# Optimization experiments

Measured on AMD Instinct MI355X. Metric: run time of the kernel, lower is better.

Reference implementation:

```python
import jax, jax.numpy as jnp
import numpy as np

K = 64          # number of instance ids (0 = background, skipped)
MARGIN = 1.0    # TripletMarginLoss margin
EPS = 1e-6      # torch pairwise_distance eps (added to the difference)
NCAND = 16      # random negative candidates per instance


def setup_inputs() -> dict:
    key = jax.random.key(0)
    k1, k2 = jax.random.split(key)
    sem_logits = jax.random.normal(k1, (4, 19, 1024, 1024), dtype=jnp.float32)
    instance_mask = jax.random.randint(k2, (1024, 1024), 0, K, dtype=jnp.int32)
    return {"sem_logits": sem_logits, "instance_mask": instance_mask}


def reference(sem_logits, instance_mask):
    B, C, H, W = sem_logits.shape
    HW = H * W
    sem_flat = sem_logits.reshape(B * C, HW)           # [BC, HW]
    mask_flat = instance_mask.reshape(HW)
    ar = jnp.arange(HW, dtype=jnp.int32)

    # first and second pixel (row-major order) of each instance id, vectorized
    first = jax.ops.segment_min(ar, mask_flat, num_segments=K)   # int32 max if empty
    ar2 = jnp.where(ar == first[mask_flat], jnp.int32(HW), ar)
    second = jax.ops.segment_min(ar2, mask_flat, num_segments=K)
    counts = jax.ops.segment_sum(jnp.ones_like(ar), mask_flat, num_segments=K)

    ids = jnp.arange(K, dtype=jnp.int32)
    valid = (counts >= 2) & (ids != 0)

    # random negative: first candidate pixel whose instance id differs
    cand = jax.random.randint(jax.random.key(1), (K, NCAND), 0, HW, dtype=jnp.int32)
    cand_ok = mask_flat[cand] != ids[:, None]
    pick = jnp.argmax(cand_ok, axis=1)
    neg = cand[jnp.arange(K), pick]

    f = jnp.clip(first, 0, HW - 1)
    s = jnp.clip(second, 0, HW - 1)

    a = sem_flat[:, f].T    # [K, B*C] anchor vectors (flattened per-pixel logits)
    p = sem_flat[:, s].T    # positive
    n = sem_flat[:, neg].T  # negative

    d_ap = jnp.linalg.norm(a - p + EPS, axis=1)
    d_an = jnp.linalg.norm(a - n + EPS, axis=1)
    per_inst = jnp.maximum(d_ap - d_an + MARGIN, 0.0)

    cnt = jnp.sum(valid)
    total = jnp.sum(jnp.where(valid, per_inst, 0.0))
    return jnp.where(cnt > 0, total / cnt, jnp.float32(0.0))
```

## Files before the change

### kernel.cpp

```cpp
#include <hip/hip_runtime.h>
#include <stdint.h>

#define HW        (1024 * 1024)
#define KIDS      64
#define NCANDS    16
#define BCC       76
#define EPSF      1e-6f
#define MARGINF   1.0f
#define SENTINEL  0x7FFFFFFF

#define JAX_PARTITIONABLE 1

__device__ __forceinline__ uint32_t rotl32(uint32_t v, int r) {
    return (v << r) | (v >> (32 - r));
}

__device__ void threefry2x32(uint32_t k0, uint32_t k1, uint32_t x0, uint32_t x1,
                             uint32_t* o0, uint32_t* o1) {
    const uint32_t ks2 = k0 ^ k1 ^ 0x1BD11BDAu;
    const int R0[4] = {13, 15, 26, 6};
    const int R1[4] = {17, 29, 16, 24};
    x0 += k0; x1 += k1;
#pragma unroll
    for (int i = 0; i < 4; i++) { x0 += x1; x1 = rotl32(x1, R0[i]); x1 ^= x0; }
    x0 += k1; x1 += ks2 + 1u;
#pragma unroll
    for (int i = 0; i < 4; i++) { x0 += x1; x1 = rotl32(x1, R1[i]); x1 ^= x0; }
    x0 += ks2; x1 += k0 + 2u;
#pragma unroll
    for (int i = 0; i < 4; i++) { x0 += x1; x1 = rotl32(x1, R0[i]); x1 ^= x0; }
    x0 += k0; x1 += k1 + 3u;
#pragma unroll
    for (int i = 0; i < 4; i++) { x0 += x1; x1 = rotl32(x1, R1[i]); x1 ^= x0; }
    x0 += k1; x1 += ks2 + 4u;
#pragma unroll
    for (int i = 0; i < 4; i++) { x0 += x1; x1 = rotl32(x1, R0[i]); x1 ^= x0; }
    x0 += ks2; x1 += k0 + 5u;
    *o0 = x0; *o1 = x1;
}

__device__ uint32_t jax_cand_bits(uint32_t j) {
#if JAX_PARTITIONABLE
    uint32_t k2a, k2b;
    threefry2x32(0u, 1u, 0u, 1u, &k2a, &k2b);
    uint32_t b1, b2;
    threefry2x32(k2a, k2b, 0u, j, &b1, &b2);
    return b1 ^ b2;
#else
    uint32_t a0, a1, b0, b1;
    threefry2x32(0u, 1u, 0u, 2u, &a0, &a1);
    threefry2x32(0u, 1u, 1u, 3u, &b0, &b1);
    uint32_t k2a = a1, k2b = b1;
    uint32_t r0, r1;
    if (j < 512u) { threefry2x32(k2a, k2b, j, j + 512u, &r0, &r1); return r0; }
    else          { threefry2x32(k2a, k2b, j - 512u, j, &r0, &r1); return r1; }
#endif
}

__global__ void k_init(int* g_first, int* g_second, int* g_count,
                       float* g_total, int* g_cnt) {
    int t = threadIdx.x;
    if (t < KIDS) { g_first[t] = SENTINEL; g_second[t] = SENTINEL; g_count[t] = 0; }
    if (t == 0)   { *g_total = 0.0f; *g_cnt = 0; }
}

__global__ void k_seg(const int* __restrict__ mask,
                      int* g_first, int* g_second, int* g_count) {
    __shared__ int m1[KIDS], m2[KIDS], cnt[KIDS];
    const int t = threadIdx.x;
    if (t < KIDS) { m1[t] = SENTINEL; m2[t] = SENTINEL; cnt[t] = 0; }
    __syncthreads();

    const int4* m4 = (const int4*)mask;
    const int base4 = blockIdx.x * 1024;
    int4 v[4];
#pragma unroll
    for (int c = 0; c < 4; c++) v[c] = m4[base4 + c * 256 + t];

#pragma unroll
    for (int c = 0; c < 4; c++) {
        const int pix0 = (base4 + c * 256 + t) * 4;
        const int ids[4] = {v[c].x, v[c].y, v[c].z, v[c].w};
#pragma unroll
        for (int j = 0; j < 4; j++) {
            atomicAdd(&cnt[ids[j]], 1);
            atomicMin(&m1[ids[j]], pix0 + j);
        }
    }
    __syncthreads();
#pragma unroll
    for (int c = 0; c < 4; c++) {
        const int pix0 = (base4 + c * 256 + t) * 4;
        const int ids[4] = {v[c].x, v[c].y, v[c].z, v[c].w};
#pragma unroll
        for (int j = 0; j < 4; j++) {
            if (pix0 + j != m1[ids[j]]) atomicMin(&m2[ids[j]], pix0 + j);
        }
    }
    __syncthreads();

    if (t < KIDS && cnt[t] > 0) {
        const int lm1 = m1[t];
        const int old = atomicMin(&g_first[t], lm1);
        const int disp = old > lm1 ? old : lm1;
        if (disp != SENTINEL)  atomicMin(&g_second[t], disp);
        if (m2[t] != SENTINEL) atomicMin(&g_second[t], m2[t]);
        atomicAdd(&g_count[t], cnt[t]);
    }
}

__global__ void k_triplet(const float* __restrict__ sem,
                          const int* __restrict__ mask,
                          const int* __restrict__ g_first,
                          const int* __restrict__ g_second,
                          const int* __restrict__ g_count,
                          float* g_total, int* g_cnt) {
    const int k = blockIdx.x;
    if (k == 0 || g_count[k] < 2) return;

    __shared__ int s_neg;
    __shared__ float red_ap[128], red_an[128];
    const int t = threadIdx.x;

    if (t == 0) {
        int neg = -1, first_cand = -1;
        for (int c = 0; c < NCANDS; c++) {
            const uint32_t bits = jax_cand_bits((uint32_t)(k * NCANDS + c));
            const int cand = (int)(bits & (uint32_t)(HW - 1));
            if (c == 0) first_cand = cand;
            if (neg < 0 && mask[cand] != k) neg = cand;
        }
        s_neg = (neg < 0) ? first_cand : neg;
    }
    __syncthreads();

    const int f = g_first[k], s = g_second[k], n = s_neg;
    float ap = 0.0f, an = 0.0f;
    if (t < BCC) {
        const size_t row = (size_t)t * (size_t)HW;
        const float a  = sem[row + f];
        const float p  = sem[row + s];
        const float nn = sem[row + n];
        const float d1 = a - p + EPSF;
        const float d2 = a - nn + EPSF;
        ap = d1 * d1;
        an = d2 * d2;
    }
    red_ap[t] = ap; red_an[t] = an;
    __syncthreads();
    for (int off = 64; off > 0; off >>= 1) {
        if (t < off) { red_ap[t] += red_ap[t + off]; red_an[t] += red_an[t + off]; }
        __syncthreads();
    }
    if (t == 0) {
        float per = sqrtf(red_ap[0]) - sqrtf(red_an[0]) + MARGINF;
        per = per > 0.0f ? per : 0.0f;
        atomicAdd(g_total, per);
        atomicAdd(g_cnt, 1);
    }
}

__global__ void k_final(const float* __restrict__ g_total,
                        const int* __restrict__ g_cnt, float* out) {
    const int c = *g_cnt;
    out[0] = (c > 0) ? (*g_total / (float)c) : 0.0f;
}

extern "C" void kernel_launch(void* const* d_in, const int* in_sizes, int n_in,
                              void* d_out, int out_size, void* d_ws, size_t ws_size,
                              hipStream_t stream) {
    const float* sem  = (const float*)d_in[0];
    const int*   mask = (const int*)d_in[1];
    float* out = (float*)d_out;

    int* ws = (int*)d_ws;
    int* g_first  = ws;
    int* g_second = ws + 64;
    int* g_count  = ws + 128;
    float* g_total = (float*)(ws + 192);
    int*   g_cnt   = ws + 193;

    k_init<<<1, 64, 0, stream>>>(g_first, g_second, g_count, g_total, g_cnt);
    k_seg<<<HW / 4096, 256, 0, stream>>>(mask, g_first, g_second, g_count);
    k_triplet<<<KIDS, 128, 0, stream>>>(sem, mask, g_first, g_second, g_count,
                                        g_total, g_cnt);
    k_final<<<1, 1, 0, stream>>>(g_total, g_cnt, out);
}
```

Measured before the change: 361.2 us.

## Replace global atomics with per-block partials and deterministic reductions, drop init kernel

The segment kernel now writes per-block (first, second) partial minima to workspace instead of doing global atomics and counts, so the separate init kernel can be removed. The triplet kernel merges the 256 partials per id with a two-smallest reduction, derives validity from the second index, and computes the 16 negative candidates in parallel with a wavefront ballot. The final kernel reduces per-id results with shuffles. This saves one launch and the global atomic contention, at the cost of a small extra reduction over the partials.

Measured after the change: 348.8 us. 3.4% less time.

```diff
diff --git a/kernel.cpp b/kernel.cpp
--- a/kernel.cpp
+++ b/kernel.cpp
@@ -8,6 +8,7 @@
 #define EPSF      1e-6f
 #define MARGINF   1.0f
 #define SENTINEL  0x7FFFFFFF
+#define SEGB      256
 
 #define JAX_PARTITIONABLE 1
 
@@ -57,18 +58,10 @@
 #endif
 }
 
-__global__ void k_init(int* g_first, int* g_second, int* g_count,
-                       float* g_total, int* g_cnt) {
-    int t = threadIdx.x;
-    if (t < KIDS) { g_first[t] = SENTINEL; g_second[t] = SENTINEL; g_count[t] = 0; }
-    if (t == 0)   { *g_total = 0.0f; *g_cnt = 0; }
-}
-
-__global__ void k_seg(const int* __restrict__ mask,
-                      int* g_first, int* g_second, int* g_count) {
-    __shared__ int m1[KIDS], m2[KIDS], cnt[KIDS];
+__global__ void k_seg(const int* __restrict__ mask, int2* __restrict__ part) {
+    __shared__ int m1[KIDS], m2[KIDS];
     const int t = threadIdx.x;
-    if (t < KIDS) { m1[t] = SENTINEL; m2[t] = SENTINEL; cnt[t] = 0; }
+    if (t < KIDS) { m1[t] = SENTINEL; m2[t] = SENTINEL; }
     __syncthreads();
 
     const int4* m4 = (const int4*)mask;
@@ -82,10 +75,7 @@
         const int pix0 = (base4 + c * 256 + t) * 4;
         const int ids[4] = {v[c].x, v[c].y, v[c].z, v[c].w};
 #pragma unroll
-        for (int j = 0; j < 4; j++) {
-            atomicAdd(&cnt[ids[j]], 1);
-            atomicMin(&m1[ids[j]], pix0 + j);
-        }
+        for (int j = 0; j < 4; j++) atomicMin(&m1[ids[j]], pix0 + j);
     }
     __syncthreads();
 #pragma unroll
@@ -99,42 +89,61 @@
     }
     __syncthreads();
 
-    if (t < KIDS && cnt[t] > 0) {
-        const int lm1 = m1[t];
-        const int old = atomicMin(&g_first[t], lm1);
-        const int disp = old > lm1 ? old : lm1;
-        if (disp != SENTINEL)  atomicMin(&g_second[t], disp);
-        if (m2[t] != SENTINEL) atomicMin(&g_second[t], m2[t]);
-        atomicAdd(&g_count[t], cnt[t]);
-    }
+    if (t < KIDS) part[blockIdx.x * KIDS + t] = make_int2(m1[t], m2[t]);
 }
 
 __global__ void k_triplet(const float* __restrict__ sem,
                           const int* __restrict__ mask,
-                          const int* __restrict__ g_first,
-                          const int* __restrict__ g_second,
-                          const int* __restrict__ g_count,
-                          float* g_total, int* g_cnt) {
+                          const int2* __restrict__ part,
+                          float* __restrict__ per_out,
+                          int* __restrict__ valid_out) {
     const int k = blockIdx.x;
-    if (k == 0 || g_count[k] < 2) return;
+    const int t = threadIdx.x;
+    __shared__ int s_neg;
+    __shared__ int red_lo[128], red_hi[128];
+    __shared__ float red_ap[128], red_an[128];
 
-    __shared__ int s_neg;
-    __shared__ float red_ap[128], red_an[128];
-    const int t = threadIdx.x;
+    if (t < 64) {
+        int cand = 0, ok = 0;
+        if (t < NCANDS) {
+            const uint32_t bits = jax_cand_bits((uint32_t)(k * NCANDS + t));
+            cand = (int)(bits & (uint32_t)(HW - 1));
+            ok = (mask[cand] != k) ? 1 : 0;
+        }
+        const unsigned long long bal = __ballot(ok);
+        const int pick = bal ? (__ffsll(bal) - 1) : 0;
+        const int neg = __shfl(cand, pick, 64);
+        if (t == 0) s_neg = neg;
+    }
 
-    if (t == 0) {
-        int neg = -1, first_cand = -1;
-        for (int c = 0; c < NCANDS; c++) {
-            const uint32_t bits = jax_cand_bits((uint32_t)(k * NCANDS + c));
-            const int cand = (int)(bits & (uint32_t)(HW - 1));
-            if (c == 0) first_cand = cand;
-            if (neg < 0 && mask[cand] != k) neg = cand;
+    int lo = SENTINEL, hi = SENTINEL;
+#pragma unroll
+    for (int r = 0; r < SEGB / 128; r++) {
+        const int2 pq = part[(r * 128 + t) * KIDS + k];
+        const int nlo = min(lo, pq.x);
+        const int nhi = min(max(lo, pq.x), min(hi, pq.y));
+        lo = nlo; hi = nhi;
+    }
+    red_lo[t] = lo; red_hi[t] = hi;
+    __syncthreads();
+    for (int off = 64; off > 0; off >>= 1) {
+        if (t < off) {
+            const int a1 = red_lo[t + off], a2 = red_hi[t + off];
+            const int l = red_lo[t], h = red_hi[t];
+            red_lo[t] = min(l, a1);
+            red_hi[t] = min(max(l, a1), min(h, a2));
         }
-        s_neg = (neg < 0) ? first_cand : neg;
+        __syncthreads();
     }
-    __syncthreads();
+    const int f = red_lo[0];
+    const int s = red_hi[0];
+    const bool valid = (k != 0) && (s != SENTINEL);
+    if (!valid) {
+        if (t == 0) { per_out[k] = 0.0f; valid_out[k] = 0; }
+        return;
+    }
 
-    const int f = g_first[k], s = g_second[k], n = s_neg;
+    const int n = s_neg;
     float ap = 0.0f, an = 0.0f;
     if (t < BCC) {
         const size_t row = (size_t)t * (size_t)HW;
@@ -154,16 +163,23 @@
     }
     if (t == 0) {
         float per = sqrtf(red_ap[0]) - sqrtf(red_an[0]) + MARGINF;
-        per = per > 0.0f ? per : 0.0f;
-        atomicAdd(g_total, per);
-        atomicAdd(g_cnt, 1);
+        per_out[k] = per > 0.0f ? per : 0.0f;
+        valid_out[k] = 1;
     }
 }
 
-__global__ void k_final(const float* __restrict__ g_total,
-                        const int* __restrict__ g_cnt, float* out) {
-    const int c = *g_cnt;
-    out[0] = (c > 0) ? (*g_total / (float)c) : 0.0f;
+__global__ void k_final(const float* __restrict__ per,
+                        const int* __restrict__ valid,
+                        float* __restrict__ out) {
+    const int t = threadIdx.x;
+    float v = per[t];
+    int   c = valid[t];
+#pragma unroll
+    for (int off = 32; off > 0; off >>= 1) {
+        v += __shfl_down(v, off, 64);
+        c += __shfl_down(c, off, 64);
+    }
+    if (t == 0) out[0] = (c > 0) ? (v / (float)c) : 0.0f;
 }
 
 extern "C" void kernel_launch(void* const* d_in, const int* in_sizes, int n_in,
@@ -173,16 +189,11 @@
     const int*   mask = (const int*)d_in[1];
     float* out = (float*)d_out;
 
-    int* ws = (int*)d_ws;
-    int* g_first  = ws;
-    int* g_second = ws + 64;
-    int* g_count  = ws + 128;
-    float* g_total = (float*)(ws + 192);
-    int*   g_cnt   = ws + 193;
+    int2*  part  = (int2*)d_ws;
+    float* per   = (float*)((char*)d_ws + (size_t)SEGB * KIDS * sizeof(int2));
+    int*   valid = (int*)((char*)per + KIDS * sizeof(float));
 
-    k_init<<<1, 64, 0, stream>>>(g_first, g_second, g_count, g_total, g_cnt);
-    k_seg<<<HW / 4096, 256, 0, stream>>>(mask, g_first, g_second, g_count);
-    k_triplet<<<KIDS, 128, 0, stream>>>(sem, mask, g_first, g_second, g_count,
-                                        g_total, g_cnt);
-    k_final<<<1, 1, 0, stream>>>(g_total, g_cnt, out);
+    k_seg<<<HW / 4096, 256, 0, stream>>>(mask, part);
+    k_triplet<<<KIDS, 128, 0, stream>>>(sem, mask, part, per, valid);
+    k_final<<<1, 64, 0, stream>>>(per, valid, out);
 }
```
